# Performance work log

Measured on AMD Instinct MI355X. Metric: run time of the kernel, lower is better.

Reference implementation:

```python
import jax, jax.numpy as jnp
import numpy as np

N, E = 50000, 800000
IN_F, OUT_F, H = 128, 128, 4
D = OUT_F // H  # head dim
NEG_SLOPE = 0.2
EPS = 1e-12


def setup_inputs() -> dict:
    key = jax.random.key(0)
    ks = jax.random.split(key, 10)
    s = 1.0 / np.sqrt(IN_F)
    return {
        "x": jax.random.normal(ks[0], (N, IN_F), jnp.float32),
        "W_src": jax.random.normal(ks[1], (IN_F, H * D), jnp.float32) * s,
        "b_src": jnp.zeros((H * D,), jnp.float32),
        "W_dst": jax.random.normal(ks[2], (IN_F, H * D), jnp.float32) * s,
        "b_dst": jnp.zeros((H * D,), jnp.float32),
        "attn": jax.random.normal(ks[3], (H, D), jnp.float32) * (1.0 / np.sqrt(D)),
        "out_bias": jnp.zeros((H * D,), jnp.float32),
        "ln_w": jnp.ones((OUT_F,), jnp.float32),
        "ln_b": jnp.zeros((OUT_F,), jnp.float32),
        "src": jax.random.randint(ks[4], (E,), 0, N, jnp.int32),
        "dst": jax.random.randint(ks[5], (E,), 0, N, jnp.int32),
    }


def reference(x, W_src, b_src, W_dst, b_dst, attn, out_bias, ln_w, ln_b, src, dst):
    n = x.shape[0]
    # GATv2Conv (share_weights=False): separate source/dest projections
    fs = (x @ W_src + b_src).reshape(n, H, D)  # [N,H,D]
    fd = (x @ W_dst + b_dst).reshape(n, H, D)
    # per-edge scores: e_ij = attn . leaky_relu(fs[u] + fd[v])
    e = jax.nn.leaky_relu(fs[src] + fd[dst], NEG_SLOPE)  # [E,H,D]
    logits = jnp.einsum("ehd,hd->eh", e, attn)  # [E,H]
    # edge softmax over incoming edges of each dst node
    m = jax.ops.segment_max(logits, dst, num_segments=n)  # [N,H]
    ex = jnp.exp(logits - m[dst])
    denom = jax.ops.segment_sum(ex, dst, num_segments=n)  # [N,H]
    alpha = ex / denom[dst]  # [E,H]
    # aggregate: sum_j alpha_ij * fs[j]
    msg = alpha[:, :, None] * fs[src]  # [E,H,D]
    rst = jax.ops.segment_sum(msg, dst, num_segments=n)  # [N,H,D]
    h = rst.reshape(n, H * D) + out_bias
    # LayerNorm (biased variance, eps inside sqrt)
    u = h.mean(-1, keepdims=True)
    s = jnp.mean((h - u) ** 2, -1, keepdims=True)
    h = (h - u) / jnp.sqrt(s + EPS)
    h = ln_w * h + ln_b
    # activation = elu; dropout p=0 -> identity
    return jax.nn.elu(h)
```

## Files before the change

### kernel.cpp

```cpp
#include <hip/hip_runtime.h>
#include <hip/hip_bf16.h>

constexpr int NF = 128;

using bf16x8 = __attribute__((ext_vector_type(8))) short;
using f32x4v = __attribute__((ext_vector_type(4))) float;

__device__ __forceinline__ unsigned short f2bs(float f) {
    return __builtin_bit_cast(unsigned short, __float2bfloat16(f));
}
__device__ __forceinline__ void unpack8(float4 raw, float* a) {
    unsigned u0 = __float_as_uint(raw.x);
    unsigned u1 = __float_as_uint(raw.y);
    unsigned u2 = __float_as_uint(raw.z);
    unsigned u3 = __float_as_uint(raw.w);
    a[0] = __uint_as_float(u0 << 16);
    a[1] = __uint_as_float(u0 & 0xffff0000u);
    a[2] = __uint_as_float(u1 << 16);
    a[3] = __uint_as_float(u1 & 0xffff0000u);
    a[4] = __uint_as_float(u2 << 16);
    a[5] = __uint_as_float(u2 & 0xffff0000u);
    a[6] = __uint_as_float(u3 << 16);
    a[7] = __uint_as_float(u3 & 0xffff0000u);
}

__global__ void GraphAttnLayer_70196945486348_kernel() {}

__global__ __launch_bounds__(256) void prep_kernel(
    const float* __restrict__ Wsrc, const float* __restrict__ Wdst,
    unsigned short* __restrict__ Wb,
    int* __restrict__ cnt8, int* __restrict__ state, int N8, int NB)
{
    int i = blockIdx.x * 256 + threadIdx.x;
    if (i < N8) cnt8[i] = 0;
    if (i < NB) state[i] = 0;
    if (i < 256 * NF) {
        int k   = i >> 8;
        int col = i & 255;
        float v = (col < 128) ? Wsrc[k * NF + col] : Wdst[k * NF + (col - 128)];
        Wb[col * NF + k] = f2bs(v);
    }
}

__global__ __launch_bounds__(256) void gemm_hist_kernel(
    const float* __restrict__ x,
    const unsigned short* __restrict__ Wb,
    const float* __restrict__ bsrc, const float* __restrict__ bdst,
    unsigned short* __restrict__ fs,
    float* __restrict__ fd,
    const int* __restrict__ src, const int* __restrict__ dst,
    int* __restrict__ cnt8, int* __restrict__ pack,
    int N, int E, int NGB)
{
    {
        int e = blockIdx.x * 256 + threadIdx.x;
        if (e < E) {
            int c = blockIdx.x & 7;
            int r = atomicAdd(&cnt8[c * N + dst[e]], 1);
            pack[e] = (r << 17) | src[e];
        }
    }
    if (blockIdx.x >= NGB) return;

    const int lane = threadIdx.x & 63;
    const int wave = threadIdx.x >> 6;
    const int m_base = blockIdx.x * 32;
    const int lm = lane & 15;
    const int kq = (lane >> 4) * 8;

    bf16x8 bfrag[4][4];
    float bias[4];
#pragma unroll
    for (int c = 0; c < 4; ++c) {
        int col = wave * 64 + c * 16 + lm;
        bias[c] = (col < 128) ? bsrc[col] : bdst[col - 128];
#pragma unroll
        for (int s = 0; s < 4; ++s)
            bfrag[c][s] = *(const bf16x8*)(Wb + col * NF + s * 32 + kq);
    }

    for (int r = 0; r < 2; ++r) {
        int m0 = m_base + r * 16;
        if (m0 >= N) break;
        int row = m0 + lm;
        if (row >= N) row = N - 1;
        bf16x8 afrag[4];
#pragma unroll
        for (int s = 0; s < 4; ++s) {
            const float4* xp = (const float4*)(x + (size_t)row * NF + s * 32 + kq);
            float4 xa = xp[0], xb = xp[1];
            afrag[s][0] = (short)f2bs(xa.x);
            afrag[s][1] = (short)f2bs(xa.y);
            afrag[s][2] = (short)f2bs(xa.z);
            afrag[s][3] = (short)f2bs(xa.w);
            afrag[s][4] = (short)f2bs(xb.x);
            afrag[s][5] = (short)f2bs(xb.y);
            afrag[s][6] = (short)f2bs(xb.z);
            afrag[s][7] = (short)f2bs(xb.w);
        }
#pragma unroll
        for (int c = 0; c < 4; ++c) {
            f32x4v acc = {0.f, 0.f, 0.f, 0.f};
#pragma unroll
            for (int s = 0; s < 4; ++s)
                acc = __builtin_amdgcn_mfma_f32_16x16x32_bf16(afrag[s], bfrag[c][s], acc, 0, 0, 0);
            int col = wave * 64 + c * 16 + lm;
            int cc = col & 127;
#pragma unroll
            for (int rr = 0; rr < 4; ++rr) {
                int rowd = m0 + (lane >> 4) * 4 + rr;
                if (rowd < N) {
                    float v = acc[rr] + bias[c];
                    if (col < 128) fs[(size_t)rowd * NF + cc] = f2bs(v);
                    else           fd[(size_t)rowd * NF + cc] = v;
                }
            }
        }
    }
}

__global__ __launch_bounds__(256) void scan_kernel(
    const int* __restrict__ cnt8, int* __restrict__ rowptr,
    int* __restrict__ ptr8, int* __restrict__ state, int N, int E)
{
    int b = blockIdx.x, t = threadIdx.x;
    int i = b * 256 + t;

    int v[8];
    int tot = 0;
    if (i < N) {
#pragma unroll
        for (int c = 0; c < 8; ++c) { v[c] = cnt8[c * N + i]; tot += v[c]; }
    }

    __shared__ int arr[256];
    __shared__ int s_bofs;
    arr[t] = tot;
    __syncthreads();
    for (int off = 1; off < 256; off <<= 1) {
        int u = (t >= off) ? arr[t - off] : 0;
        __syncthreads();
        arr[t] += u;
        __syncthreads();
    }
    int total = arr[255];

    if (t < 64) {
        if (t == 0) {
            int word = ((b == 0 ? 2 : 1) << 30) | total;
            atomicExch(&state[b], word);
        }
        int bofs = 0;
        if (b > 0) {
            int base = b;
            for (;;) {
                int j = base - 1 - t;
                int sv = 0, f = 1;
                if (j >= 0) {
                    sv = __hip_atomic_load(&state[j], __ATOMIC_RELAXED,
                                           __HIP_MEMORY_SCOPE_AGENT);
                    f = ((unsigned)sv) >> 30;
                }
                unsigned long long notready = __ballot(f == 0);
                if (notready) continue;
                unsigned long long has2 = __ballot(f == 2);
                if (has2) {
                    int k = (int)(__ffsll((unsigned long long)has2) - 1);
                    int val = (t <= k) ? (sv & 0x3FFFFFFF) : 0;
#pragma unroll
                    for (int off = 32; off; off >>= 1) val += __shfl_xor(val, off);
                    bofs += val;
                    break;
                } else {
                    int val = (j >= 0) ? (sv & 0x3FFFFFFF) : 0;
#pragma unroll
                    for (int off = 32; off; off >>= 1) val += __shfl_xor(val, off);
                    bofs += val;
                    base -= 64;
                }
            }
            if (t == 0) atomicExch(&state[b], (2 << 30) | (bofs + total));
        }
        if (t == 0) s_bofs = bofs;
    }
    __syncthreads();
    int bofs = s_bofs;
    int excl = arr[t] - tot + bofs;
    if (i < N) {
        rowptr[i] = excl;
        int run = excl;
#pragma unroll
        for (int c = 0; c < 8; ++c) { ptr8[i * 8 + c] = run; run += v[c]; }
    }
    if (i == 0) rowptr[N] = E;
}

__global__ __launch_bounds__(256) void scatter_kernel(
    const int* __restrict__ dst, const int* __restrict__ pack,
    const int* __restrict__ ptr8, int* __restrict__ src_sorted, int E)
{
    int idx = blockIdx.x * 256 + threadIdx.x;
    int e0 = idx * 4;
    if (e0 + 3 < E) {
        int4 d = *(const int4*)(dst + e0);
        int4 p = *(const int4*)(pack + e0);
        int c0 = ((e0 + 0) >> 8) & 7;
        int c1 = ((e0 + 1) >> 8) & 7;
        int c2 = ((e0 + 2) >> 8) & 7;
        int c3 = ((e0 + 3) >> 8) & 7;
        src_sorted[ptr8[d.x * 8 + c0] + (p.x >> 17)] = p.x & 0x1FFFF;
        src_sorted[ptr8[d.y * 8 + c1] + (p.y >> 17)] = p.y & 0x1FFFF;
        src_sorted[ptr8[d.z * 8 + c2] + (p.z >> 17)] = p.z & 0x1FFFF;
        src_sorted[ptr8[d.w * 8 + c3] + (p.w >> 17)] = p.w & 0x1FFFF;
    } else {
        for (int e = e0; e < E; ++e) {
            int p = pack[e];
            int c = (e >> 8) & 7;
            src_sorted[ptr8[dst[e] * 8 + c] + (p >> 17)] = p & 0x1FFFF;
        }
    }
}

__global__ __launch_bounds__(256) void node_kernel(
    const float4* __restrict__ fsq,
    const int* __restrict__ rowptr, const int* __restrict__ src_sorted,
    const float4* __restrict__ attn4,
    const float4* __restrict__ obias4,
    const float4* __restrict__ lnw4,
    const float4* __restrict__ lnb4,
    float4* __restrict__ out4, int N)
{
    int lane = threadIdx.x & 63;
    int es = lane >> 4;
    int g  = lane & 15;
    int n = blockIdx.x * 4 + (threadIdx.x >> 6);
    if (n >= N) return;

    float4 fda = out4[(size_t)n * 32 + g * 2];
    float4 fdb = out4[(size_t)n * 32 + g * 2 + 1];
    float4 ava = attn4[g * 2];
    float4 avb = attn4[g * 2 + 1];
    float fd[8] = {fda.x, fda.y, fda.z, fda.w, fdb.x, fdb.y, fdb.z, fdb.w};
    float av[8] = {ava.x, ava.y, ava.z, ava.w, avb.x, avb.y, avb.z, avb.w};

    int beg = rowptr[n], end = rowptr[n + 1];
    float l = 0.f;
    float ac[8] = {0.f, 0.f, 0.f, 0.f, 0.f, 0.f, 0.f, 0.f};

    for (int j = beg; j < end; j += 4) {
        int idx = j + es;
        bool valid = idx < end;
        int s = src_sorted[valid ? idx : (end - 1)];
        float4 raw = fsq[(size_t)s * 16 + g];
        float a[8];
        unpack8(raw, a);
        float p = 0.f;
#pragma unroll
        for (int d = 0; d < 8; ++d) {
            float t = a[d] + fd[d];
            t = fmaxf(t, 0.2f * t);
            p += av[d] * t;
        }
        p += __shfl_xor(p, 1);
        p += __shfl_xor(p, 2);
        float e = valid ? __expf(p) : 0.f;
        l += e;
#pragma unroll
        for (int d = 0; d < 8; ++d) ac[d] += e * a[d];
    }

    l += __shfl_xor(l, 16);
    l += __shfl_xor(l, 32);
#pragma unroll
    for (int d = 0; d < 8; ++d) {
        ac[d] += __shfl_xor(ac[d], 16);
        ac[d] += __shfl_xor(ac[d], 32);
    }

    float rl = (l > 0.f) ? (1.f / l) : 0.f;
    float4 oba = obias4[g * 2];
    float4 obb = obias4[g * 2 + 1];
    float ob[8] = {oba.x, oba.y, oba.z, oba.w, obb.x, obb.y, obb.z, obb.w};
    float h[8];
    float s1 = 0.f, s2 = 0.f;
#pragma unroll
    for (int d = 0; d < 8; ++d) {
        h[d] = ac[d] * rl + ob[d];
        s1 += h[d];
        s2 += h[d] * h[d];
    }
    s1 += __shfl_xor(s1, 1); s2 += __shfl_xor(s2, 1);
    s1 += __shfl_xor(s1, 2); s2 += __shfl_xor(s2, 2);
    s1 += __shfl_xor(s1, 4); s2 += __shfl_xor(s2, 4);
    s1 += __shfl_xor(s1, 8); s2 += __shfl_xor(s2, 8);

    float u = s1 * (1.f / NF);
    float var = s2 * (1.f / NF) - u * u;
    float rstd = rsqrtf(fmaxf(var, 0.f) + 1e-12f);
    float4 gwa = lnw4[g * 2], gwb = lnw4[g * 2 + 1];
    float4 gba = lnb4[g * 2], gbb = lnb4[g * 2 + 1];
    float gw[8] = {gwa.x, gwa.y, gwa.z, gwa.w, gwb.x, gwb.y, gwb.z, gwb.w};
    float gb[8] = {gba.x, gba.y, gba.z, gba.w, gbb.x, gbb.y, gbb.z, gbb.w};
    float z[8];
#pragma unroll
    for (int d = 0; d < 8; ++d) {
        float y = gw[d] * ((h[d] - u) * rstd) + gb[d];
        z[d] = (y > 0.f) ? y : (__expf(y) - 1.f);
    }
    if (es == 0) {
        out4[(size_t)n * 32 + g * 2]     = make_float4(z[0], z[1], z[2], z[3]);
        out4[(size_t)n * 32 + g * 2 + 1] = make_float4(z[4], z[5], z[6], z[7]);
    }
}

extern "C" void kernel_launch(void* const* d_in, const int* in_sizes, int n_in,
                              void* d_out, int out_size, void* d_ws, size_t ws_size,
                              hipStream_t stream)
{
    const float* x    = (const float*)d_in[0];
    const float* Wsrc = (const float*)d_in[1];
    const float* bsrc = (const float*)d_in[2];
    const float* Wdst = (const float*)d_in[3];
    const float* bdst = (const float*)d_in[4];
    const float4* attn4 = (const float4*)d_in[5];
    const float4* obias4= (const float4*)d_in[6];
    const float4* lnw4  = (const float4*)d_in[7];
    const float4* lnb4  = (const float4*)d_in[8];
    const int* src = (const int*)d_in[9];
    const int* dst = (const int*)d_in[10];
    int N = in_sizes[0] / NF;
    int E = in_sizes[9];
    int NB = (N + 255) / 256;
    int N8 = N * 8;

    int* cnt8 = (int*)d_ws;
    int* state = cnt8 + N8;
    int* rowptr = state + NB;
    int* ptr8 = rowptr + (N + 1);
    int* pack = ptr8 + N8;
    int* srcs = pack + E;
    unsigned short* Wb = (unsigned short*)(srcs + E);
    unsigned short* fs = Wb + 256 * NF;

    int NGB = (N + 31) / 32;
    int GB  = (E + 255) / 256;
    if (GB < NGB) GB = NGB;
    int PB = (N8 + 255) / 256;

    prep_kernel<<<PB, 256, 0, stream>>>(Wsrc, Wdst, Wb, cnt8, state, N8, NB);
    gemm_hist_kernel<<<GB, 256, 0, stream>>>(
        x, Wb, bsrc, bdst, fs, (float*)d_out, src, dst, cnt8, pack, N, E, NGB);
    scan_kernel<<<NB, 256, 0, stream>>>(cnt8, rowptr, ptr8, state, N, E);
    scatter_kernel<<<(E / 4 + 255) / 256, 256, 0, stream>>>(dst, pack, ptr8, srcs, E);
    node_kernel<<<(N + 3) / 4, 256, 0, stream>>>(
        (const float4*)fs, rowptr, srcs, attn4, obias4, lnw4, lnb4,
        (float4*)d_out, N);
}
```

Measured before the change: 216.6 us.

## Partition edge-count atomics by XCD and store sorted sources as 16-bit

```diff
diff --git a/kernel.cpp b/kernel.cpp
--- a/kernel.cpp
+++ b/kernel.cpp
@@ -23,6 +23,9 @@
     a[6] = __uint_as_float(u3 << 16);
     a[7] = __uint_as_float(u3 & 0xffff0000u);
 }
+__device__ __forceinline__ unsigned xcd_id() {
+    return __builtin_amdgcn_s_getreg(63508) & 7u;
+}
 
 __global__ void GraphAttnLayer_70196945486348_kernel() {}
 
@@ -55,9 +58,11 @@
     {
         int e = blockIdx.x * 256 + threadIdx.x;
         if (e < E) {
-            int c = blockIdx.x & 7;
-            int r = atomicAdd(&cnt8[c * N + dst[e]], 1);
-            pack[e] = (r << 17) | src[e];
+            unsigned c = xcd_id();
+            int r = __hip_atomic_fetch_add(&cnt8[c * N + dst[e]], 1,
+                                           __ATOMIC_RELAXED,
+                                           __HIP_MEMORY_SCOPE_WORKGROUP);
+            pack[e] = (int)((c << 29) | ((unsigned)r << 16) | (unsigned)src[e]);
         }
     }
     if (blockIdx.x >= NGB) return;
@@ -197,33 +202,36 @@
 
 __global__ __launch_bounds__(256) void scatter_kernel(
     const int* __restrict__ dst, const int* __restrict__ pack,
-    const int* __restrict__ ptr8, int* __restrict__ src_sorted, int E)
+    const int* __restrict__ ptr8, unsigned short* __restrict__ src_sorted,
+    int E)
 {
     int idx = blockIdx.x * 256 + threadIdx.x;
     int e0 = idx * 4;
     if (e0 + 3 < E) {
         int4 d = *(const int4*)(dst + e0);
         int4 p = *(const int4*)(pack + e0);
-        int c0 = ((e0 + 0) >> 8) & 7;
-        int c1 = ((e0 + 1) >> 8) & 7;
-        int c2 = ((e0 + 2) >> 8) & 7;
-        int c3 = ((e0 + 3) >> 8) & 7;
-        src_sorted[ptr8[d.x * 8 + c0] + (p.x >> 17)] = p.x & 0x1FFFF;
-        src_sorted[ptr8[d.y * 8 + c1] + (p.y >> 17)] = p.y & 0x1FFFF;
-        src_sorted[ptr8[d.z * 8 + c2] + (p.z >> 17)] = p.z & 0x1FFFF;
-        src_sorted[ptr8[d.w * 8 + c3] + (p.w >> 17)] = p.w & 0x1FFFF;
+        unsigned px = (unsigned)p.x, py = (unsigned)p.y,
+                 pz = (unsigned)p.z, pw = (unsigned)p.w;
+        src_sorted[ptr8[d.x * 8 + (px >> 29)] + ((px >> 16) & 0x1FFF)] =
+            (unsigned short)(px & 0xFFFF);
+        src_sorted[ptr8[d.y * 8 + (py >> 29)] + ((py >> 16) & 0x1FFF)] =
+            (unsigned short)(py & 0xFFFF);
+        src_sorted[ptr8[d.z * 8 + (pz >> 29)] + ((pz >> 16) & 0x1FFF)] =
+            (unsigned short)(pz & 0xFFFF);
+        src_sorted[ptr8[d.w * 8 + (pw >> 29)] + ((pw >> 16) & 0x1FFF)] =
+            (unsigned short)(pw & 0xFFFF);
     } else {
         for (int e = e0; e < E; ++e) {
-            int p = pack[e];
-            int c = (e >> 8) & 7;
-            src_sorted[ptr8[dst[e] * 8 + c] + (p >> 17)] = p & 0x1FFFF;
+            unsigned p = (unsigned)pack[e];
+            src_sorted[ptr8[dst[e] * 8 + (p >> 29)] + ((p >> 16) & 0x1FFF)] =
+                (unsigned short)(p & 0xFFFF);
         }
     }
 }
 
 __global__ __launch_bounds__(256) void node_kernel(
     const float4* __restrict__ fsq,
-    const int* __restrict__ rowptr, const int* __restrict__ src_sorted,
+    const int* __restrict__ rowptr, const unsigned short* __restrict__ src_sorted,
     const float4* __restrict__ attn4,
     const float4* __restrict__ obias4,
     const float4* __restrict__ lnw4,
@@ -338,8 +346,8 @@
     int* rowptr = state + NB;
     int* ptr8 = rowptr + (N + 1);
     int* pack = ptr8 + N8;
-    int* srcs = pack + E;
-    unsigned short* Wb = (unsigned short*)(srcs + E);
+    unsigned short* srcs = (unsigned short*)(pack + E);
+    unsigned short* Wb = srcs + ((E + 1) & ~1);
     unsigned short* fs = Wb + 256 * NF;
 
     int NGB = (N + 31) / 32;
```

New measurement: 215.3 us. No clear change (-0.6%).
